# Optimization experiments

Measured on AMD Instinct MI355X. Metric: run time of the kernel, lower is better.

Reference implementation:

```python
import jax, jax.numpy as jnp
import numpy as np

TEMP = 0.5
ALPHA, BETA, GAMMA, LAMB = 1e-3, 5e-4, 1e-3, 5e-6
IMG = 1024.0  # img_metas img_shape (H_img, W_img)
LN_EPS = 1e-5


def setup_inputs() -> dict:
    key = jax.random.key(0)
    ks = jax.random.split(key, 20)
    N, C, H, W, NB = 8, 256, 128, 128, 20
    preds_S = jax.random.normal(ks[0], (N, C, H, W), jnp.float32)
    preds_T = jax.random.normal(ks[1], (N, C, H, W), jnp.float32)
    # valid boxes (tl_x, tl_y, br_x, br_y) in pixel coords within [0, IMG]
    raw = jax.random.uniform(ks[2], (N, NB, 4), jnp.float32)
    x1 = raw[..., 0] * 0.7 * IMG
    y1 = raw[..., 1] * 0.7 * IMG
    x2 = jnp.minimum(x1 + (0.05 + raw[..., 2] * 0.25) * IMG, IMG)
    y2 = jnp.minimum(y1 + (0.05 + raw[..., 3] * 0.25) * IMG, IMG)
    gt_bboxes = jnp.stack([x1, y1, x2, y2], axis=-1)
    s = 1.0 / np.sqrt(C)
    s2 = 1.0 / np.sqrt(C // 2)
    mk = lambda k, shape, sc: jax.random.normal(k, shape, jnp.float32) * sc
    return {
        'preds_S': preds_S, 'preds_T': preds_T, 'gt_bboxes': gt_bboxes,
        'w_ms': mk(ks[3], (C,), s), 'b_ms': jnp.zeros((), jnp.float32),
        'w_mt': mk(ks[4], (C,), s), 'b_mt': jnp.zeros((), jnp.float32),
        'w1_s': mk(ks[5], (C // 2, C), s), 'b1_s': jnp.zeros((C // 2,), jnp.float32),
        'g_s': jnp.ones((C // 2,), jnp.float32), 'be_s': jnp.zeros((C // 2,), jnp.float32),
        'w2_s': mk(ks[6], (C, C // 2), s2), 'b2_s': jnp.zeros((C,), jnp.float32),
        'w1_t': mk(ks[7], (C // 2, C), s), 'b1_t': jnp.zeros((C // 2,), jnp.float32),
        'g_t': jnp.ones((C // 2,), jnp.float32), 'be_t': jnp.zeros((C // 2,), jnp.float32),
        'w2_t': mk(ks[8], (C, C // 2), s2), 'b2_t': jnp.zeros((C,), jnp.float32),
    }


def _attention(x):
    # x: [N,C,H,W] -> S_att [N,H,W], C_att [N,C]
    N, C, H, W = x.shape
    v = jnp.abs(x)
    fea = v.mean(axis=1)                                   # [N,H,W]
    S = (H * W) * jax.nn.softmax((fea / TEMP).reshape(N, -1), axis=1)
    ch = v.mean(axis=(2, 3))                               # [N,C]
    Ca = C * jax.nn.softmax(ch / TEMP, axis=1)
    return S.reshape(N, H, W), Ca


def _masks(gt, H, W):
    # gt: [N,nb,4] pixel coords; box-rasterized scatter-max foreground mask
    wmin = jnp.floor(gt[..., 0] / IMG * W)
    wmax = jnp.ceil(gt[..., 2] / IMG * W)
    hmin = jnp.floor(gt[..., 1] / IMG * H)
    hmax = jnp.ceil(gt[..., 3] / IMG * H)
    area = 1.0 / ((hmax + 1.0 - hmin) * (wmax + 1.0 - wmin))  # [N,nb]
    hs = jnp.arange(H, dtype=jnp.float32)[None, None, :, None]
    ws = jnp.arange(W, dtype=jnp.float32)[None, None, None, :]
    inb = (hs >= hmin[:, :, None, None]) & (hs <= hmax[:, :, None, None]) \
        & (ws >= wmin[:, :, None, None]) & (ws <= wmax[:, :, None, None])
    Mask_fg = jnp.where(inb, area[:, :, None, None], 0.0).max(axis=1)  # [N,H,W]
    Mask_bg = jnp.where(Mask_fg > 0, 0.0, 1.0)
    sbg = Mask_bg.sum(axis=(1, 2), keepdims=True)
    Mask_bg = jnp.where(sbg > 0, Mask_bg / sbg, Mask_bg)
    return Mask_fg, Mask_bg


def _spatial_pool(x, w, b):
    N, C, H, W = x.shape
    cm = jnp.einsum('nchw,c->nhw', x, w) + b
    sm = jax.nn.softmax(cm.reshape(N, -1), axis=1).reshape(N, H, W)
    return jnp.einsum('nchw,nhw->nc', x, sm)               # [N,C]


def _channel_add(ctx, w1, b1, g, be, w2, b2):
    y = ctx @ w1.T + b1                                    # [N,C/2]
    m = y.mean(axis=1, keepdims=True)
    v = y.var(axis=1, keepdims=True)
    y = (y - m) / jnp.sqrt(v + LN_EPS) * g + be
    y = jax.nn.relu(y)
    return y @ w2.T + b2                                   # [N,C]


def reference(preds_S, preds_T, gt_bboxes, w_ms, b_ms, w_mt, b_mt,
              w1_s, b1_s, g_s, be_s, w2_s, b2_s,
              w1_t, b1_t, g_t, be_t, w2_t, b2_t):
    N, C, H, W = preds_S.shape
    S_t, C_t = _attention(preds_T)
    S_s, C_s = _attention(preds_S)
    Mask_fg, Mask_bg = _masks(gt_bboxes, H, W)
    # feature losses: (fg_s - fg_t) = (S - T) * sqrt(S_t)*sqrt(C_t)*sqrt(mask)
    wgt = jnp.sqrt(S_t)[:, None] * jnp.sqrt(C_t)[:, :, None, None]
    d = (preds_S - preds_T) * wgt
    fg_loss = jnp.sum((d * jnp.sqrt(Mask_fg)[:, None]) ** 2) / N
    bg_loss = jnp.sum((d * jnp.sqrt(Mask_bg)[:, None]) ** 2) / N
    mask_loss = jnp.sum(jnp.abs(C_s - C_t)) / N + jnp.sum(jnp.abs(S_s - S_t)) / N
    ctx_s = _spatial_pool(preds_S, w_ms, b_ms)
    ctx_t = _spatial_pool(preds_T, w_mt, b_mt)
    add_s = _channel_add(ctx_s, w1_s, b1_s, g_s, be_s, w2_s, b2_s)
    add_t = _channel_add(ctx_t, w1_t, b1_t, g_t, be_t, w2_t, b2_t)
    rd = (preds_S + add_s[:, :, None, None]) - (preds_T + add_t[:, :, None, None])
    rela_loss = jnp.sum(rd ** 2) / N
    return ALPHA * fg_loss + BETA * bg_loss + GAMMA * mask_loss + LAMB * rela_loss
```

## Files before the change

kernel.cpp:

```cpp
#include <hip/hip_runtime.h>
#include <math.h>

#define NN    8
#define CC    256
#define HWHW  16384
#define NBOX  20
#define HALF  131072

constexpr float C_ALPHA = 1e-3f, C_BETA = 5e-4f, C_GAMMA = 1e-3f, C_LAMB = 5e-6f;
constexpr float C_LN_EPS = 1e-5f;

#define OFF_FEA_S   0
#define OFF_FEA_T   262144
#define OFF_CM_S    524288
#define OFF_CM_T    786432
#define OFF_MFG     1048576
#define OFF_CHS     1179648
#define OFF_CHT     1181696
#define OFF_DSUM    1183744
#define OFF_CTXS    1185792
#define OFF_CTXT    1187840
#define OFF_BG      1189888
#define OFF_SCAL    1189896
#define OFF_CATT    1189904
#define OFF_STATS   1191952
#define OFF_MXP     1192016
#define OFF_ZP      1192528
#define OFF_RELAP   1193040

__device__ __forceinline__ float dpp_wave_sum(float x) {
#define DPPADD(ctrl, rm) \
  x += __int_as_float(__builtin_amdgcn_update_dpp(0, __float_as_int(x), ctrl, rm, 0xf, true));
  DPPADD(0x111, 0xf)
  DPPADD(0x112, 0xf)
  DPPADD(0x114, 0xf)
  DPPADD(0x118, 0xf)
  DPPADD(0x142, 0xa)
  DPPADD(0x143, 0xc)
#undef DPPADD
  return x;
}

__device__ __forceinline__ float dpp_wave_max(float x) {
#define DPPMAX(ctrl, rm) { \
  int r_ = __builtin_amdgcn_update_dpp(__float_as_int(x), __float_as_int(x), ctrl, rm, 0xf, false); \
  x = fmaxf(x, __int_as_float(r_)); }
  DPPMAX(0x111, 0xf)
  DPPMAX(0x112, 0xf)
  DPPMAX(0x114, 0xf)
  DPPMAX(0x118, 0xf)
  DPPMAX(0x142, 0xa)
  DPPMAX(0x143, 0xc)
#undef DPPMAX
  return x;
}

__device__ __forceinline__ float block_sum256(float v, float* sm) {
  int tid = threadIdx.x;
  v = dpp_wave_sum(v);
  if ((tid & 63) == 63) sm[tid >> 6] = v;
  __syncthreads();
  float r = sm[0] + sm[1] + sm[2] + sm[3];
  __syncthreads();
  return r;
}

__device__ __forceinline__ float block_max256(float v, float* sm) {
  int tid = threadIdx.x;
  v = dpp_wave_max(v);
  if ((tid & 63) == 63) sm[tid >> 6] = v;
  __syncthreads();
  float r = fmaxf(fmaxf(sm[0], sm[1]), fmaxf(sm[2], sm[3]));
  __syncthreads();
  return r;
}

__global__ __launch_bounds__(512, 2) void k1_pass1(
    const float* __restrict__ S, const float* __restrict__ T,
    const float* __restrict__ w_ms, const float* __restrict__ w_mt,
    float* __restrict__ ws) {
  int tid = threadIdx.x;
  int lane = tid & 63, sl = tid >> 6;
  int pb = blockIdx.x, cs = blockIdx.y, n = blockIdx.z;
  int pix0 = pb * 256 + lane * 4;
  int ch0 = cs * 128 + sl * 16;

  __shared__ float l_wS[128], l_wT[128];
  __shared__ float f_feaS[256], f_feaT[256], f_cmS[256], f_cmT[256];
  __shared__ float l_chS[128], l_chT[128], l_D[128];
  __shared__ float l_sq[8];

  if (tid < 128) {
    l_wS[tid] = w_ms[cs * 128 + tid];
    l_wT[tid] = w_mt[cs * 128 + tid];
  }
  if (tid < 256) {
    f_feaS[tid] = 0.f; f_feaT[tid] = 0.f; f_cmS[tid] = 0.f; f_cmT[tid] = 0.f;
  }
  __syncthreads();

  const float* baseS = S + (size_t)(n * CC + ch0) * HWHW + pix0;
  const float* baseT = T + (size_t)(n * CC + ch0) * HWHW + pix0;

  float fS[4] = {0.f, 0.f, 0.f, 0.f}, fT[4] = {0.f, 0.f, 0.f, 0.f};
  float cS[4] = {0.f, 0.f, 0.f, 0.f}, cT[4] = {0.f, 0.f, 0.f, 0.f};
  float sq = 0.f;

#define PROC1(c, s4, t4, wS_, wT_) { \
    float asx = fabsf(s4.x), asy = fabsf(s4.y), asz = fabsf(s4.z), asw = fabsf(s4.w); \
    float atx = fabsf(t4.x), aty = fabsf(t4.y), atz = fabsf(t4.z), atw = fabsf(t4.w); \
    fS[0] += asx; fS[1] += asy; fS[2] += asz; fS[3] += asw; \
    fT[0] += atx; fT[1] += aty; fT[2] += atz; fT[3] += atw; \
    chS[c] = (asx + asy) + (asz + asw); \
    chT[c] = (atx + aty) + (atz + atw); \
    cS[0] = fmaf(s4.x, wS_, cS[0]); cS[1] = fmaf(s4.y, wS_, cS[1]); \
    cS[2] = fmaf(s4.z, wS_, cS[2]); cS[3] = fmaf(s4.w, wS_, cS[3]); \
    cT[0] = fmaf(t4.x, wT_, cT[0]); cT[1] = fmaf(t4.y, wT_, cT[1]); \
    cT[2] = fmaf(t4.z, wT_, cT[2]); cT[3] = fmaf(t4.w, wT_, cT[3]); \
    float dx = s4.x - t4.x, dy = s4.y - t4.y, dz = s4.z - t4.z, dw = s4.w - t4.w; \
    sq = fmaf(dx, dx, sq); sq = fmaf(dy, dy, sq); \
    sq = fmaf(dz, dz, sq); sq = fmaf(dw, dw, sq); \
    D[c] = (dx + dy) + (dz + dw); }

#pragma unroll 1
  for (int cg = 0; cg < 4; cg++) {
    const float* bS = baseS + (size_t)(cg * 4) * HWHW;
    const float* bT = baseT + (size_t)(cg * 4) * HWHW;
    float4 s0 = *(const float4*)(bS + (size_t)0 * HWHW);
    float4 s1 = *(const float4*)(bS + (size_t)1 * HWHW);
    float4 s2 = *(const float4*)(bS + (size_t)2 * HWHW);
    float4 s3 = *(const float4*)(bS + (size_t)3 * HWHW);
    float4 t0 = *(const float4*)(bT + (size_t)0 * HWHW);
    float4 t1 = *(const float4*)(bT + (size_t)1 * HWHW);
    float4 t2 = *(const float4*)(bT + (size_t)2 * HWHW);
    float4 t3 = *(const float4*)(bT + (size_t)3 * HWHW);
    float wS0 = l_wS[sl * 16 + cg * 4 + 0], wT0 = l_wT[sl * 16 + cg * 4 + 0];
    float wS1 = l_wS[sl * 16 + cg * 4 + 1], wT1 = l_wT[sl * 16 + cg * 4 + 1];
    float wS2 = l_wS[sl * 16 + cg * 4 + 2], wT2 = l_wT[sl * 16 + cg * 4 + 2];
    float wS3 = l_wS[sl * 16 + cg * 4 + 3], wT3 = l_wT[sl * 16 + cg * 4 + 3];
    float chS[4], chT[4], D[4];
    PROC1(0, s0, t0, wS0, wT0)
    PROC1(1, s1, t1, wS1, wT1)
    PROC1(2, s2, t2, wS2, wT2)
    PROC1(3, s3, t3, wS3, wT3)
#pragma unroll
    for (int c = 0; c < 4; c++) {
      float a = dpp_wave_sum(chS[c]);
      float b = dpp_wave_sum(chT[c]);
      float d = dpp_wave_sum(D[c]);
      if (lane == 63) {
        l_chS[sl * 16 + cg * 4 + c] = a;
        l_chT[sl * 16 + cg * 4 + c] = b;
        l_D[sl * 16 + cg * 4 + c]   = d;
      }
    }
  }
#undef PROC1

  atomicAdd(&f_feaS[lane * 4 + 0], fS[0]); atomicAdd(&f_feaS[lane * 4 + 1], fS[1]);
  atomicAdd(&f_feaS[lane * 4 + 2], fS[2]); atomicAdd(&f_feaS[lane * 4 + 3], fS[3]);
  atomicAdd(&f_feaT[lane * 4 + 0], fT[0]); atomicAdd(&f_feaT[lane * 4 + 1], fT[1]);
  atomicAdd(&f_feaT[lane * 4 + 2], fT[2]); atomicAdd(&f_feaT[lane * 4 + 3], fT[3]);
  atomicAdd(&f_cmS[lane * 4 + 0], cS[0]); atomicAdd(&f_cmS[lane * 4 + 1], cS[1]);
  atomicAdd(&f_cmS[lane * 4 + 2], cS[2]); atomicAdd(&f_cmS[lane * 4 + 3], cS[3]);
  atomicAdd(&f_cmT[lane * 4 + 0], cT[0]); atomicAdd(&f_cmT[lane * 4 + 1], cT[1]);
  atomicAdd(&f_cmT[lane * 4 + 2], cT[2]); atomicAdd(&f_cmT[lane * 4 + 3], cT[3]);

  sq = dpp_wave_sum(sq);
  if (lane == 63) l_sq[sl] = sq;
  __syncthreads();

  if (tid < 256) {
    int gp = cs * HALF + n * HWHW + pb * 256 + tid;
    ws[OFF_FEA_S + gp] = f_feaS[tid];
    ws[OFF_FEA_T + gp] = f_feaT[tid];
    ws[OFF_CM_S + gp]  = f_cmS[tid];
    ws[OFF_CM_T + gp]  = f_cmT[tid];
  }
  if (tid < 128) {
    int co = n * CC + cs * 128 + tid;
    atomicAdd(&ws[OFF_CHS + co],  l_chS[tid]);
    atomicAdd(&ws[OFF_CHT + co],  l_chT[tid]);
    atomicAdd(&ws[OFF_DSUM + co], l_D[tid]);
  }
  if (tid == 0) {
    float t = 0.f;
#pragma unroll
    for (int i = 0; i < 8; i++) t += l_sq[i];
    atomicAdd(&ws[OFF_SCAL + 0], t);
  }
}

__global__ __launch_bounds__(256) void k2B_maskstats(const float* __restrict__ gt,
                                                     float* __restrict__ ws) {
  int tid = threadIdx.x;
  int pbB = blockIdx.x, n = blockIdx.y;
  int pix0 = pbB * 1024 + tid * 4;

  __shared__ float bx[NBOX][5];
  __shared__ float l_bg[4];
  __shared__ float sm[4];

  if (tid < NBOX) {
    const float* g = gt + (n * NBOX + tid) * 4;
    float wmin = floorf(g[0] * 0.125f);
    float hmin = floorf(g[1] * 0.125f);
    float wmax = ceilf(g[2] * 0.125f);
    float hmax = ceilf(g[3] * 0.125f);
    bx[tid][0] = wmin; bx[tid][1] = hmin; bx[tid][2] = wmax; bx[tid][3] = hmax;
    bx[tid][4] = 1.0f / ((hmax + 1.0f - hmin) * (wmax + 1.0f - wmin));
  }
  __syncthreads();

  float best[4] = {0.f, 0.f, 0.f, 0.f};
#pragma unroll
  for (int b = 0; b < NBOX; b++) {
    float wmin = bx[b][0], hmin = bx[b][1], wmax = bx[b][2], hmax = bx[b][3];
    float ar = bx[b][4];
#pragma unroll
    for (int j = 0; j < 4; j++) {
      int pix = pix0 + j;
      float hf = (float)(pix >> 7), wf = (float)(pix & 127);
      bool in = (hf >= hmin) && (hf <= hmax) && (wf >= wmin) && (wf <= wmax);
      best[j] = in ? fmaxf(best[j], ar) : best[j];
    }
  }
  float4 bo;
  bo.x = best[0]; bo.y = best[1]; bo.z = best[2]; bo.w = best[3];
  *(float4*)&ws[OFF_MFG + n * HWHW + pix0] = bo;

  float bg = (best[0] > 0.f ? 0.f : 1.f) + (best[1] > 0.f ? 0.f : 1.f) +
             (best[2] > 0.f ? 0.f : 1.f) + (best[3] > 0.f ? 0.f : 1.f);
  bg = dpp_wave_sum(bg);
  if ((tid & 63) == 63) l_bg[tid >> 6] = bg;
  __syncthreads();
  if (tid == 0) atomicAdd(&ws[OFF_BG + n], l_bg[0] + l_bg[1] + l_bg[2] + l_bg[3]);

  int gp = n * HWHW + pix0;
  const int   offs[4]   = {OFF_FEA_S, OFF_FEA_T, OFF_CM_S, OFF_CM_T};
  const float scales[4] = {1.0f / 128.0f, 1.0f / 128.0f, 1.0f, 1.0f};
#pragma unroll
  for (int a = 0; a < 4; a++) {
    float4 v0 = *(const float4*)&ws[offs[a] + gp];
    float4 v1 = *(const float4*)&ws[offs[a] + HALF + gp];
    float sc = scales[a];
    float vx = (v0.x + v1.x) * sc, vy = (v0.y + v1.y) * sc;
    float vz = (v0.z + v1.z) * sc, vw = (v0.w + v1.w) * sc;
    float mx = fmaxf(fmaxf(vx, vy), fmaxf(vz, vw));
    mx = block_max256(mx, sm);
    float z = expf(vx - mx) + expf(vy - mx) + expf(vz - mx) + expf(vw - mx);
    z = block_sum256(z, sm);
    if (tid == 0) {
      ws[OFF_MXP + a * 128 + n * 16 + pbB] = mx;
      ws[OFF_ZP + a * 128 + n * 16 + pbB]  = z;
    }
  }
}

__global__ __launch_bounds__(256) void kC_stats2(float* __restrict__ ws) {
  int tid = threadIdx.x, n = blockIdx.x;
  __shared__ float sm[4];

  float chS = ws[OFF_CHS + n * CC + tid];
  float chT = ws[OFF_CHT + n * CC + tid];

  float lS = chS * (1.0f / 8192.0f), lT = chT * (1.0f / 8192.0f);
  float mS = block_max256(lS, sm);
  float mT = block_max256(lT, sm);
  float eS = expf(lS - mS), eT = expf(lT - mT);
  float ZS = block_sum256(eS, sm);
  float ZT = block_sum256(eT, sm);
  float cattS = (float)CC * eS / ZS;
  float cattT = (float)CC * eT / ZT;
  ws[OFF_CATT + n * CC + tid] = cattT;
  float mml = block_sum256(fabsf(cattS - cattT), sm);
  if (tid == 0) atomicAdd(&ws[OFF_SCAL + 2], mml);

  if (tid < 4) {
    int a = tid;
    float m = -1e30f;
    for (int i = 0; i < 16; i++)
      m = fmaxf(m, ws[OFF_MXP + a * 128 + n * 16 + i]);
    float Z = 0.f;
    for (int i = 0; i < 16; i++)
      Z += ws[OFF_ZP + a * 128 + n * 16 + i] *
           expf(ws[OFF_MXP + a * 128 + n * 16 + i] - m);
    ws[OFF_STATS + n * 8 + 2 * a]     = m;
    ws[OFF_STATS + n * 8 + 2 * a + 1] = Z;
  }
}

__global__ __launch_bounds__(512, 2) void k4_pass2(
    const float* __restrict__ S, const float* __restrict__ T,
    float* __restrict__ ws) {
  int tid = threadIdx.x;
  int lane = tid & 63, sl = tid >> 6;
  int pb = blockIdx.x, cs = blockIdx.y, n = blockIdx.z;
  int pix0 = pb * 256 + lane * 4;
  int ch0 = cs * 128 + sl * 16;

  __shared__ float l_catt[128];
  __shared__ float wcombL[256], smsL[256], smtL[256];
  __shared__ float l_cs[128], l_ct[128], l_c[8];

  if (tid < 128) l_catt[tid] = ws[OFF_CATT + n * CC + cs * 128 + tid];
  if (tid < 64) {
    float mxFS = ws[OFF_STATS + n * 8 + 0], ZFS = ws[OFF_STATS + n * 8 + 1];
    float mxFT = ws[OFF_STATS + n * 8 + 2], ZFT = ws[OFF_STATS + n * 8 + 3];
    float mxCS = ws[OFF_STATS + n * 8 + 4], ZCS = ws[OFF_STATS + n * 8 + 5];
    float mxCT = ws[OFF_STATS + n * 8 + 6], ZCT = ws[OFF_STATS + n * 8 + 7];
    float bgc  = ws[OFF_BG + n];
    int gp = n * HWHW + pb * 256 + tid * 4;
    float4 fS0 = *(const float4*)&ws[OFF_FEA_S + gp];
    float4 fS1 = *(const float4*)&ws[OFF_FEA_S + HALF + gp];
    float4 fT0 = *(const float4*)&ws[OFF_FEA_T + gp];
    float4 fT1 = *(const float4*)&ws[OFF_FEA_T + HALF + gp];
    float4 cS0 = *(const float4*)&ws[OFF_CM_S + gp];
    float4 cS1 = *(const float4*)&ws[OFF_CM_S + HALF + gp];
    float4 cT0 = *(const float4*)&ws[OFF_CM_T + gp];
    float4 cT1 = *(const float4*)&ws[OFF_CM_T + HALF + gp];
    float4 mf = *(const float4*)&ws[OFF_MFG + gp];
    float fSa[4] = {fS0.x + fS1.x, fS0.y + fS1.y, fS0.z + fS1.z, fS0.w + fS1.w};
    float fTa[4] = {fT0.x + fT1.x, fT0.y + fT1.y, fT0.z + fT1.z, fT0.w + fT1.w};
    float cSa[4] = {cS0.x + cS1.x, cS0.y + cS1.y, cS0.z + cS1.z, cS0.w + cS1.w};
    float cTa[4] = {cT0.x + cT1.x, cT0.y + cT1.y, cT0.z + cT1.z, cT0.w + cT1.w};
    float mfa[4] = {mf.x, mf.y, mf.z, mf.w};
    float macc = 0.f;
#pragma unroll
    for (int j = 0; j < 4; j++) {
      float pT = expf(fTa[j] * (1.0f / 128.0f) - mxFT) / ZFT;
      float pS = expf(fSa[j] * (1.0f / 128.0f) - mxFS) / ZFS;
      float Satt = (float)HWHW * pT;
      float mbg = (mfa[j] > 0.f) ? 0.f : ((bgc > 0.f) ? 1.0f / bgc : 1.0f);
      wcombL[tid * 4 + j] = Satt * (C_ALPHA * mfa[j] + C_BETA * mbg);
      smsL[tid * 4 + j] = expf(cSa[j] - mxCS) / ZCS;
      smtL[tid * 4 + j] = expf(cTa[j] - mxCT) / ZCT;
      macc += fabsf(pS - pT);
    }
    macc = dpp_wave_sum(macc);
    if (tid == 63 && cs == 0) atomicAdd(&ws[OFF_SCAL + 2], macc * (float)HWHW);
  }
  __syncthreads();

  float4 sms = *(const float4*)&smsL[lane * 4];
  float4 smt = *(const float4*)&smtL[lane * 4];
  float4 wcb = *(const float4*)&wcombL[lane * 4];

  const float* baseS = S + (size_t)(n * CC + ch0) * HWHW + pix0;
  const float* baseT = T + (size_t)(n * CC + ch0) * HWHW + pix0;

  float aw[4] = {0.f, 0.f, 0.f, 0.f};

#define PROC2(c, s4, t4, ca_) { \
    float dx = s4.x - t4.x, dy = s4.y - t4.y, dz = s4.z - t4.z, dw = s4.w - t4.w; \
    aw[0] = fmaf(dx * dx, ca_, aw[0]); aw[1] = fmaf(dy * dy, ca_, aw[1]); \
    aw[2] = fmaf(dz * dz, ca_, aw[2]); aw[3] = fmaf(dw * dw, ca_, aw[3]); \
    ctxS[c] = fmaf(s4.x, sms.x, fmaf(s4.y, sms.y, fmaf(s4.z, sms.z, s4.w * sms.w))); \
    ctxT[c] = fmaf(t4.x, smt.x, fmaf(t4.y, smt.y, fmaf(t4.z, smt.z, t4.w * smt.w))); }

#pragma unroll 1
  for (int cg = 0; cg < 4; cg++) {
    const float* bS = baseS + (size_t)(cg * 4) * HWHW;
    const float* bT = baseT + (size_t)(cg * 4) * HWHW;
    float4 s0 = *(const float4*)(bS + (size_t)0 * HWHW);
    float4 s1 = *(const float4*)(bS + (size_t)1 * HWHW);
    float4 s2 = *(const float4*)(bS + (size_t)2 * HWHW);
    float4 s3 = *(const float4*)(bS + (size_t)3 * HWHW);
    float4 t0 = *(const float4*)(bT + (size_t)0 * HWHW);
    float4 t1 = *(const float4*)(bT + (size_t)1 * HWHW);
    float4 t2 = *(const float4*)(bT + (size_t)2 * HWHW);
    float4 t3 = *(const float4*)(bT + (size_t)3 * HWHW);
    float ca0 = l_catt[sl * 16 + cg * 4 + 0];
    float ca1 = l_catt[sl * 16 + cg * 4 + 1];
    float ca2 = l_catt[sl * 16 + cg * 4 + 2];
    float ca3 = l_catt[sl * 16 + cg * 4 + 3];
    float ctxS[4], ctxT[4];
    PROC2(0, s0, t0, ca0)
    PROC2(1, s1, t1, ca1)
    PROC2(2, s2, t2, ca2)
    PROC2(3, s3, t3, ca3)
#pragma unroll
    for (int c = 0; c < 4; c++) {
      float xs = dpp_wave_sum(ctxS[c]);
      float xt = dpp_wave_sum(ctxT[c]);
      if (lane == 63) {
        l_cs[sl * 16 + cg * 4 + c] = xs;
        l_ct[sl * 16 + cg * 4 + c] = xt;
      }
    }
  }
#undef PROC2

  float contrib = fmaf(aw[0], wcb.x, fmaf(aw[1], wcb.y, fmaf(aw[2], wcb.z, aw[3] * wcb.w)));
  contrib = dpp_wave_sum(contrib);
  if (lane == 63) l_c[sl] = contrib;
  __syncthreads();

  if (tid < 128) {
    int co = n * CC + cs * 128 + tid;
    atomicAdd(&ws[OFF_CTXS + co], l_cs[tid]);
    atomicAdd(&ws[OFF_CTXT + co], l_ct[tid]);
  }
  if (tid == 0) {
    float t = 0.f;
#pragma unroll
    for (int i = 0; i < 8; i++) t += l_c[i];
    atomicAdd(&ws[OFF_SCAL + 1], t);
  }
}

__global__ __launch_bounds__(512) void k5_mlp(
    const float* __restrict__ w1_s, const float* __restrict__ b1_s,
    const float* __restrict__ g_s,  const float* __restrict__ be_s,
    const float* __restrict__ w1_t, const float* __restrict__ b1_t,
    const float* __restrict__ g_t,  const float* __restrict__ be_t,
    const float* __restrict__ w2_s, const float* __restrict__ b2_s,
    const float* __restrict__ w2_t, const float* __restrict__ b2_t,
    float* __restrict__ ws) {
  int tid = threadIdx.x, n = blockIdx.x;
  int lane = tid & 63;
  __shared__ float ctxS[CC], ctxT[CC], ysh[128], yth[128];
  __shared__ float red[4], smr[8];

  if (tid < 256)      ctxS[tid] = ws[OFF_CTXS + n * CC + tid];
  else                ctxT[tid - 256] = ws[OFF_CTXT + n * CC + (tid - 256)];
  __syncthreads();

  int st = (tid >> 7) & 1, j = tid & 127;
  float acc = 0.f;
  if (tid < 256) {
    const float* w1 = st ? w1_t : w1_s;
    const float* b1 = st ? b1_t : b1_s;
    const float* ctx = st ? ctxT : ctxS;
    acc = b1[j];
    const float* wr = w1 + j * CC;
#pragma unroll 8
    for (int c = 0; c < CC; c += 4) {
      float4 w = *(const float4*)(wr + c);
      acc = fmaf(w.x, ctx[c], acc);
      acc = fmaf(w.y, ctx[c + 1], acc);
      acc = fmaf(w.z, ctx[c + 2], acc);
      acc = fmaf(w.w, ctx[c + 3], acc);
    }
  }

  float v = dpp_wave_sum(acc);
  if (tid < 256 && lane == 63) red[tid >> 6] = v;
  __syncthreads();
  int grp = tid >> 7;
  float mean = 0.f;
  if (tid < 256) mean = (red[grp * 2] + red[grp * 2 + 1]) * (1.0f / 128.0f);
  __syncthreads();
  float dm = acc - mean;
  v = dpp_wave_sum(dm * dm);
  if (tid < 256 && lane == 63) red[tid >> 6] = v;
  __syncthreads();
  if (tid < 256) {
    float var = (red[grp * 2] + red[grp * 2 + 1]) * (1.0f / 128.0f);
    const float* g  = st ? g_t  : g_s;
    const float* be = st ? be_t : be_s;
    float q = dm * (1.0f / sqrtf(var + C_LN_EPS)) * g[j] + be[j];
    q = q > 0.f ? q : 0.f;
    if (st == 0) ysh[j] = q;
    else         yth[j] = q;
  }
  __syncthreads();

  float rp = 0.f;
  if (tid < 256) {
    int c = tid;
    float es = b2_s[c], et = b2_t[c];
    const float* w2sr = w2_s + c * 128;
    const float* w2tr = w2_t + c * 128;
#pragma unroll 8
    for (int jj = 0; jj < 128; jj += 4) {
      float4 a = *(const float4*)(w2sr + jj);
      float4 b = *(const float4*)(w2tr + jj);
      es = fmaf(a.x, ysh[jj], es); es = fmaf(a.y, ysh[jj + 1], es);
      es = fmaf(a.z, ysh[jj + 2], es); es = fmaf(a.w, ysh[jj + 3], es);
      et = fmaf(b.x, yth[jj], et); et = fmaf(b.y, yth[jj + 1], et);
      et = fmaf(b.z, yth[jj + 2], et); et = fmaf(b.w, yth[jj + 3], et);
    }
    float e = es - et;
    rp = 2.0f * e * ws[OFF_DSUM + n * CC + c] + (float)HWHW * e * e;
  }
  rp = dpp_wave_sum(rp);
  if (lane == 63) smr[tid >> 6] = rp;
  __syncthreads();
  if (tid == 0) {
    float t = 0.f;
#pragma unroll
    for (int i = 0; i < 8; i++) t += smr[i];
    ws[OFF_RELAP + n] = t;
  }
}

__global__ __launch_bounds__(64) void k5c_final(float* __restrict__ ws,
                                                float* __restrict__ out) {
  int lane = threadIdx.x;
  float r = (lane < NN) ? ws[OFF_RELAP + lane] : 0.f;
  r = dpp_wave_sum(r);
  if (lane == 63) {
    float rela = ws[OFF_SCAL + 0] + r;
    out[0] = (ws[OFF_SCAL + 1] + C_GAMMA * ws[OFF_SCAL + 2] + C_LAMB * rela) *
             (1.0f / (float)NN);
  }
}

extern "C" void kernel_launch(void* const* d_in, const int* in_sizes, int n_in,
                              void* d_out, int out_size, void* d_ws, size_t ws_size,
                              hipStream_t stream) {
  const float* S    = (const float*)d_in[0];
  const float* T    = (const float*)d_in[1];
  const float* gt   = (const float*)d_in[2];
  const float* w_ms = (const float*)d_in[3];
  const float* w_mt = (const float*)d_in[5];
  const float* w1_s = (const float*)d_in[7];
  const float* b1_s = (const float*)d_in[8];
  const float* g_s  = (const float*)d_in[9];
  const float* be_s = (const float*)d_in[10];
  const float* w2_s = (const float*)d_in[11];
  const float* b2_s = (const float*)d_in[12];
  const float* w1_t = (const float*)d_in[13];
  const float* b1_t = (const float*)d_in[14];
  const float* g_t  = (const float*)d_in[15];
  const float* be_t = (const float*)d_in[16];
  const float* w2_t = (const float*)d_in[17];
  const float* b2_t = (const float*)d_in[18];
  float* ws = (float*)d_ws;
  float* out = (float*)d_out;

  hipMemsetAsync(ws + OFF_CHS, 0, 10256 * sizeof(float), stream);

  k1_pass1<<<dim3(64, 2, 8), dim3(512), 0, stream>>>(S, T, w_ms, w_mt, ws);
  k2B_maskstats<<<dim3(16, 8), dim3(256), 0, stream>>>(gt, ws);
  kC_stats2<<<dim3(8), dim3(256), 0, stream>>>(ws);
  k4_pass2<<<dim3(64, 2, 8), dim3(512), 0, stream>>>(S, T, ws);
  k5_mlp<<<dim3(8), dim3(512), 0, stream>>>(w1_s, b1_s, g_s, be_s,
                                            w1_t, b1_t, g_t, be_t,
                                            w2_s, b2_s, w2_t, b2_t, ws);
  k5c_final<<<dim3(1), dim3(64), 0, stream>>>(ws, out);
}
```

Measured before the change: 398.8 us.

## Cut launch count: fold memset into mask kernel, merge stats, last-block final reduce

Replaces the memset with zeroing inside a new mask-rasterization kernel that runs before pass1. It merges the two small stats kernels into one per-image kernel that runs an online softmax over all pixels. It also drops the final kernel by having the last MLP block, detected with an atomic counter, compute the output. The goal is to remove three launches and their serialization gaps. In exchange the merged stats kernel uses only 8 blocks with serial loops over 16K pixels and four maps, which may lengthen the critical path.

```diff
diff --git a/kernel.cpp b/kernel.cpp
--- a/kernel.cpp
+++ b/kernel.cpp
@@ -24,9 +24,10 @@
 #define OFF_SCAL    1189896
 #define OFF_CATT    1189904
 #define OFF_STATS   1191952
-#define OFF_MXP     1192016
-#define OFF_ZP      1192528
 #define OFF_RELAP   1193040
+#define OFF_BGP     1193048
+#define OFF_MML     1193176
+#define ZERO_SPAN   10256
 
 __device__ __forceinline__ float dpp_wave_sum(float x) {
 #define DPPADD(ctrl, rm) \
@@ -73,6 +74,55 @@
   float r = fmaxf(fmaxf(sm[0], sm[1]), fmaxf(sm[2], sm[3]));
   __syncthreads();
   return r;
+}
+
+__global__ __launch_bounds__(256) void k0_maskzero(const float* __restrict__ gt,
+                                                   float* __restrict__ ws) {
+  int tid = threadIdx.x;
+  int pbB = blockIdx.x, n = blockIdx.y;
+  int pix0 = pbB * 1024 + tid * 4;
+
+  int gi = (n * 16 + pbB) * 256 + tid;
+  if (gi < ZERO_SPAN) ws[OFF_CHS + gi] = 0.f;
+
+  __shared__ float bx[NBOX][5];
+  __shared__ float l_bg[4];
+
+  if (tid < NBOX) {
+    const float* g = gt + (n * NBOX + tid) * 4;
+    float wmin = floorf(g[0] * 0.125f);
+    float hmin = floorf(g[1] * 0.125f);
+    float wmax = ceilf(g[2] * 0.125f);
+    float hmax = ceilf(g[3] * 0.125f);
+    bx[tid][0] = wmin; bx[tid][1] = hmin; bx[tid][2] = wmax; bx[tid][3] = hmax;
+    bx[tid][4] = 1.0f / ((hmax + 1.0f - hmin) * (wmax + 1.0f - wmin));
+  }
+  __syncthreads();
+
+  float best[4] = {0.f, 0.f, 0.f, 0.f};
+#pragma unroll
+  for (int b = 0; b < NBOX; b++) {
+    float wmin = bx[b][0], hmin = bx[b][1], wmax = bx[b][2], hmax = bx[b][3];
+    float ar = bx[b][4];
+#pragma unroll
+    for (int j = 0; j < 4; j++) {
+      int pix = pix0 + j;
+      float hf = (float)(pix >> 7), wf = (float)(pix & 127);
+      bool in = (hf >= hmin) && (hf <= hmax) && (wf >= wmin) && (wf <= wmax);
+      best[j] = in ? fmaxf(best[j], ar) : best[j];
+    }
+  }
+  float4 bo;
+  bo.x = best[0]; bo.y = best[1]; bo.z = best[2]; bo.w = best[3];
+  *(float4*)&ws[OFF_MFG + n * HWHW + pix0] = bo;
+
+  float bg = (best[0] > 0.f ? 0.f : 1.f) + (best[1] > 0.f ? 0.f : 1.f) +
+             (best[2] > 0.f ? 0.f : 1.f) + (best[3] > 0.f ? 0.f : 1.f);
+  bg = dpp_wave_sum(bg);
+  if ((tid & 63) == 63) l_bg[tid >> 6] = bg;
+  __syncthreads();
+  if (tid == 0)
+    ws[OFF_BGP + n * 16 + pbB] = l_bg[0] + l_bg[1] + l_bg[2] + l_bg[3];
 }
 
 __global__ __launch_bounds__(512, 2) void k1_pass1(
@@ -191,79 +241,64 @@
   }
 }
 
-__global__ __launch_bounds__(256) void k2B_maskstats(const float* __restrict__ gt,
-                                                     float* __restrict__ ws) {
-  int tid = threadIdx.x;
-  int pbB = blockIdx.x, n = blockIdx.y;
-  int pix0 = pbB * 1024 + tid * 4;
-
-  __shared__ float bx[NBOX][5];
-  __shared__ float l_bg[4];
+__global__ __launch_bounds__(256) void k2C_stats(float* __restrict__ ws) {
+  int tid = threadIdx.x, n = blockIdx.x;
+  int lane = tid & 63;
   __shared__ float sm[4];
-
-  if (tid < NBOX) {
-    const float* g = gt + (n * NBOX + tid) * 4;
-    float wmin = floorf(g[0] * 0.125f);
-    float hmin = floorf(g[1] * 0.125f);
-    float wmax = ceilf(g[2] * 0.125f);
-    float hmax = ceilf(g[3] * 0.125f);
-    bx[tid][0] = wmin; bx[tid][1] = hmin; bx[tid][2] = wmax; bx[tid][3] = hmax;
-    bx[tid][4] = 1.0f / ((hmax + 1.0f - hmin) * (wmax + 1.0f - wmin));
-  }
-  __syncthreads();
-
-  float best[4] = {0.f, 0.f, 0.f, 0.f};
-#pragma unroll
-  for (int b = 0; b < NBOX; b++) {
-    float wmin = bx[b][0], hmin = bx[b][1], wmax = bx[b][2], hmax = bx[b][3];
-    float ar = bx[b][4];
-#pragma unroll
-    for (int j = 0; j < 4; j++) {
-      int pix = pix0 + j;
-      float hf = (float)(pix >> 7), wf = (float)(pix & 127);
-      bool in = (hf >= hmin) && (hf <= hmax) && (wf >= wmin) && (wf <= wmax);
-      best[j] = in ? fmaxf(best[j], ar) : best[j];
-    }
-  }
-  float4 bo;
-  bo.x = best[0]; bo.y = best[1]; bo.z = best[2]; bo.w = best[3];
-  *(float4*)&ws[OFF_MFG + n * HWHW + pix0] = bo;
-
-  float bg = (best[0] > 0.f ? 0.f : 1.f) + (best[1] > 0.f ? 0.f : 1.f) +
-             (best[2] > 0.f ? 0.f : 1.f) + (best[3] > 0.f ? 0.f : 1.f);
-  bg = dpp_wave_sum(bg);
-  if ((tid & 63) == 63) l_bg[tid >> 6] = bg;
-  __syncthreads();
-  if (tid == 0) atomicAdd(&ws[OFF_BG + n], l_bg[0] + l_bg[1] + l_bg[2] + l_bg[3]);
-
-  int gp = n * HWHW + pix0;
+  __shared__ float wm[4], wz[4];
+
+  if (tid == 0) {
+    float b = 0.f;
+    for (int i = 0; i < 16; i++) b += ws[OFF_BGP + n * 16 + i];
+    ws[OFF_BG + n] = b;
+  }
+
   const int   offs[4]   = {OFF_FEA_S, OFF_FEA_T, OFF_CM_S, OFF_CM_T};
   const float scales[4] = {1.0f / 128.0f, 1.0f / 128.0f, 1.0f, 1.0f};
-#pragma unroll
+#pragma unroll 1
   for (int a = 0; a < 4; a++) {
-    float4 v0 = *(const float4*)&ws[offs[a] + gp];
-    float4 v1 = *(const float4*)&ws[offs[a] + HALF + gp];
+    float m = -1e30f, z = 0.f;
+    int base = offs[a] + n * HWHW;
     float sc = scales[a];
-    float vx = (v0.x + v1.x) * sc, vy = (v0.y + v1.y) * sc;
-    float vz = (v0.z + v1.z) * sc, vw = (v0.w + v1.w) * sc;
-    float mx = fmaxf(fmaxf(vx, vy), fmaxf(vz, vw));
-    mx = block_max256(mx, sm);
-    float z = expf(vx - mx) + expf(vy - mx) + expf(vz - mx) + expf(vw - mx);
-    z = block_sum256(z, sm);
+    for (int k = 0; k < 16; k++) {
+      int i = k * 1024 + tid * 4;
+      float4 v0 = *(const float4*)&ws[base + i];
+      float4 v1 = *(const float4*)&ws[base + HALF + i];
+      float vv[4] = {(v0.x + v1.x) * sc, (v0.y + v1.y) * sc,
+                     (v0.z + v1.z) * sc, (v0.w + v1.w) * sc};
+#pragma unroll
+      for (int j = 0; j < 4; j++) {
+        float v = vv[j];
+        float mn = fmaxf(m, v);
+        z = z * expf(m - mn) + expf(v - mn);
+        m = mn;
+      }
+    }
+#pragma unroll
+    for (int d = 1; d < 64; d <<= 1) {
+      float m2 = __shfl_xor(m, d);
+      float z2 = __shfl_xor(z, d);
+      float mn = fmaxf(m, m2);
+      z = z * expf(m - mn) + z2 * expf(m2 - mn);
+      m = mn;
+    }
+    if (lane == 0) { wm[tid >> 6] = m; wz[tid >> 6] = z; }
+    __syncthreads();
     if (tid == 0) {
-      ws[OFF_MXP + a * 128 + n * 16 + pbB] = mx;
-      ws[OFF_ZP + a * 128 + n * 16 + pbB]  = z;
-    }
-  }
-}
-
-__global__ __launch_bounds__(256) void kC_stats2(float* __restrict__ ws) {
-  int tid = threadIdx.x, n = blockIdx.x;
-  __shared__ float sm[4];
+      float M = wm[0], Z = wz[0];
+      for (int w = 1; w < 4; w++) {
+        float mn = fmaxf(M, wm[w]);
+        Z = Z * expf(M - mn) + wz[w] * expf(wm[w] - mn);
+        M = mn;
+      }
+      ws[OFF_STATS + n * 8 + 2 * a]     = M;
+      ws[OFF_STATS + n * 8 + 2 * a + 1] = Z;
+    }
+    __syncthreads();
+  }
 
   float chS = ws[OFF_CHS + n * CC + tid];
   float chT = ws[OFF_CHT + n * CC + tid];
-
   float lS = chS * (1.0f / 8192.0f), lT = chT * (1.0f / 8192.0f);
   float mS = block_max256(lS, sm);
   float mT = block_max256(lT, sm);
@@ -274,20 +309,7 @@
   float cattT = (float)CC * eT / ZT;
   ws[OFF_CATT + n * CC + tid] = cattT;
   float mml = block_sum256(fabsf(cattS - cattT), sm);
-  if (tid == 0) atomicAdd(&ws[OFF_SCAL + 2], mml);
-
-  if (tid < 4) {
-    int a = tid;
-    float m = -1e30f;
-    for (int i = 0; i < 16; i++)
-      m = fmaxf(m, ws[OFF_MXP + a * 128 + n * 16 + i]);
-    float Z = 0.f;
-    for (int i = 0; i < 16; i++)
-      Z += ws[OFF_ZP + a * 128 + n * 16 + i] *
-           expf(ws[OFF_MXP + a * 128 + n * 16 + i] - m);
-    ws[OFF_STATS + n * 8 + 2 * a]     = m;
-    ws[OFF_STATS + n * 8 + 2 * a + 1] = Z;
-  }
+  if (tid == 0) ws[OFF_MML + n] = mml;
 }
 
 __global__ __launch_bounds__(512, 2) void k4_pass2(
@@ -409,14 +431,14 @@
   }
 }
 
-__global__ __launch_bounds__(512) void k5_mlp(
+__global__ __launch_bounds__(512) void k5F_mlp(
     const float* __restrict__ w1_s, const float* __restrict__ b1_s,
     const float* __restrict__ g_s,  const float* __restrict__ be_s,
     const float* __restrict__ w1_t, const float* __restrict__ b1_t,
     const float* __restrict__ g_t,  const float* __restrict__ be_t,
     const float* __restrict__ w2_s, const float* __restrict__ b2_s,
     const float* __restrict__ w2_t, const float* __restrict__ b2_t,
-    float* __restrict__ ws) {
+    float* __restrict__ ws, float* __restrict__ out) {
   int tid = threadIdx.x, n = blockIdx.x;
   int lane = tid & 63;
   __shared__ float ctxS[CC], ctxT[CC], ysh[128], yth[128];
@@ -487,23 +509,26 @@
   rp = dpp_wave_sum(rp);
   if (lane == 63) smr[tid >> 6] = rp;
   __syncthreads();
+
   if (tid == 0) {
     float t = 0.f;
 #pragma unroll
     for (int i = 0; i < 8; i++) t += smr[i];
     ws[OFF_RELAP + n] = t;
-  }
-}
-
-__global__ __launch_bounds__(64) void k5c_final(float* __restrict__ ws,
-                                                float* __restrict__ out) {
-  int lane = threadIdx.x;
-  float r = (lane < NN) ? ws[OFF_RELAP + lane] : 0.f;
-  r = dpp_wave_sum(r);
-  if (lane == 63) {
-    float rela = ws[OFF_SCAL + 0] + r;
-    out[0] = (ws[OFF_SCAL + 1] + C_GAMMA * ws[OFF_SCAL + 2] + C_LAMB * rela) *
-             (1.0f / (float)NN);
+    __threadfence();
+    int old = atomicAdd((int*)&ws[OFF_SCAL + 3], 1);
+    if (old == NN - 1) {
+      __threadfence();
+      float relp = 0.f, mml = ws[OFF_SCAL + 2];
+#pragma unroll
+      for (int i = 0; i < NN; i++) {
+        relp += ws[OFF_RELAP + i];
+        mml  += ws[OFF_MML + i];
+      }
+      float rela = ws[OFF_SCAL + 0] + relp;
+      out[0] = (ws[OFF_SCAL + 1] + C_GAMMA * mml + C_LAMB * rela) *
+               (1.0f / (float)NN);
+    }
   }
 }
 
@@ -530,14 +555,11 @@
   float* ws = (float*)d_ws;
   float* out = (float*)d_out;
 
-  hipMemsetAsync(ws + OFF_CHS, 0, 10256 * sizeof(float), stream);
-
+  k0_maskzero<<<dim3(16, 8), dim3(256), 0, stream>>>(gt, ws);
   k1_pass1<<<dim3(64, 2, 8), dim3(512), 0, stream>>>(S, T, w_ms, w_mt, ws);
-  k2B_maskstats<<<dim3(16, 8), dim3(256), 0, stream>>>(gt, ws);
-  kC_stats2<<<dim3(8), dim3(256), 0, stream>>>(ws);
+  k2C_stats<<<dim3(8), dim3(256), 0, stream>>>(ws);
   k4_pass2<<<dim3(64, 2, 8), dim3(512), 0, stream>>>(S, T, ws);
-  k5_mlp<<<dim3(8), dim3(512), 0, stream>>>(w1_s, b1_s, g_s, be_s,
-                                            w1_t, b1_t, g_t, be_t,
-                                            w2_s, b2_s, w2_t, b2_t, ws);
-  k5c_final<<<dim3(1), dim3(64), 0, stream>>>(ws, out);
-}
+  k5F_mlp<<<dim3(8), dim3(512), 0, stream>>>(w1_s, b1_s, g_s, be_s,
+                                             w1_t, b1_t, g_t, be_t,
+                                             w2_s, b2_s, w2_t, b2_t, ws, out);
+}
```

Measured after the change: 428.3 us. 1.07x slower.

## Fold memset into mask kernel and fuse final reduction into MLP kernel

Applied to the files above, without the earlier changes.

Replaces the hipMemsetAsync with a k0 kernel that zeroes the workspace and also rasterizes the foreground mask, moving that work ahead of pass1. Background counts and per-sample mask losses now go to per-block slots instead of atomics, and the final scalar combine moves into the MLP kernel through a last-block-done atomic counter, dropping one launch. The aim is to cut launch and serialization overhead between small kernels. The counter at SCAL+3 lies inside the zeroed span, so it resets every call.

```diff
diff --git a/kernel.cpp b/kernel.cpp
--- a/kernel.cpp
+++ b/kernel.cpp
@@ -27,6 +27,9 @@
 #define OFF_MXP     1192016
 #define OFF_ZP      1192528
 #define OFF_RELAP   1193040
+#define OFF_BGP     1193048
+#define OFF_MML     1193176
+#define ZERO_SPAN   10256
 
 __device__ __forceinline__ float dpp_wave_sum(float x) {
 #define DPPADD(ctrl, rm) \
@@ -73,6 +76,51 @@
   float r = fmaxf(fmaxf(sm[0], sm[1]), fmaxf(sm[2], sm[3]));
   __syncthreads();
   return r;
+}
+
+__global__ __launch_bounds__(256) void k0_maskzero(const float* __restrict__ gt,
+                                                   float* __restrict__ ws) {
+  int tid = threadIdx.x;
+  int pbB = blockIdx.x, n = blockIdx.y;
+  int pix0 = pbB * 1024 + tid * 4;
+  int gi = (n * 16 + pbB) * 256 + tid;
+  if (gi < ZERO_SPAN) ws[OFF_CHS + gi] = 0.f;
+
+  __shared__ float bx[NBOX][5];
+  __shared__ float l_bg[4];
+  if (tid < NBOX) {
+    const float* g = gt + (n * NBOX + tid) * 4;
+    float wmin = floorf(g[0] * 0.125f);
+    float hmin = floorf(g[1] * 0.125f);
+    float wmax = ceilf(g[2] * 0.125f);
+    float hmax = ceilf(g[3] * 0.125f);
+    bx[tid][0] = wmin; bx[tid][1] = hmin; bx[tid][2] = wmax; bx[tid][3] = hmax;
+    bx[tid][4] = 1.0f / ((hmax + 1.0f - hmin) * (wmax + 1.0f - wmin));
+  }
+  __syncthreads();
+  float best[4] = {0.f, 0.f, 0.f, 0.f};
+#pragma unroll
+  for (int b = 0; b < NBOX; b++) {
+    float wmin = bx[b][0], hmin = bx[b][1], wmax = bx[b][2], hmax = bx[b][3];
+    float ar = bx[b][4];
+#pragma unroll
+    for (int j = 0; j < 4; j++) {
+      int pix = pix0 + j;
+      float hf = (float)(pix >> 7), wf = (float)(pix & 127);
+      bool in = (hf >= hmin) && (hf <= hmax) && (wf >= wmin) && (wf <= wmax);
+      best[j] = in ? fmaxf(best[j], ar) : best[j];
+    }
+  }
+  float4 bo;
+  bo.x = best[0]; bo.y = best[1]; bo.z = best[2]; bo.w = best[3];
+  *(float4*)&ws[OFF_MFG + n * HWHW + pix0] = bo;
+  float bg = (best[0] > 0.f ? 0.f : 1.f) + (best[1] > 0.f ? 0.f : 1.f) +
+             (best[2] > 0.f ? 0.f : 1.f) + (best[3] > 0.f ? 0.f : 1.f);
+  bg = dpp_wave_sum(bg);
+  if ((tid & 63) == 63) l_bg[tid >> 6] = bg;
+  __syncthreads();
+  if (tid == 0)
+    ws[OFF_BGP + n * 16 + pbB] = l_bg[0] + l_bg[1] + l_bg[2] + l_bg[3];
 }
 
 __global__ __launch_bounds__(512, 2) void k1_pass1(
@@ -123,9 +171,9 @@
     D[c] = (dx + dy) + (dz + dw); }
 
 #pragma unroll 1
-  for (int cg = 0; cg < 4; cg++) {
-    const float* bS = baseS + (size_t)(cg * 4) * HWHW;
-    const float* bT = baseT + (size_t)(cg * 4) * HWHW;
+  for (int cg4 = 0; cg4 < 4; cg4++) {
+    const float* bS = baseS + (size_t)(cg4 * 4) * HWHW;
+    const float* bT = baseT + (size_t)(cg4 * 4) * HWHW;
     float4 s0 = *(const float4*)(bS + (size_t)0 * HWHW);
     float4 s1 = *(const float4*)(bS + (size_t)1 * HWHW);
     float4 s2 = *(const float4*)(bS + (size_t)2 * HWHW);
@@ -134,10 +182,10 @@
     float4 t1 = *(const float4*)(bT + (size_t)1 * HWHW);
     float4 t2 = *(const float4*)(bT + (size_t)2 * HWHW);
     float4 t3 = *(const float4*)(bT + (size_t)3 * HWHW);
-    float wS0 = l_wS[sl * 16 + cg * 4 + 0], wT0 = l_wT[sl * 16 + cg * 4 + 0];
-    float wS1 = l_wS[sl * 16 + cg * 4 + 1], wT1 = l_wT[sl * 16 + cg * 4 + 1];
-    float wS2 = l_wS[sl * 16 + cg * 4 + 2], wT2 = l_wT[sl * 16 + cg * 4 + 2];
-    float wS3 = l_wS[sl * 16 + cg * 4 + 3], wT3 = l_wT[sl * 16 + cg * 4 + 3];
+    float wS0 = l_wS[sl * 16 + cg4 * 4 + 0], wT0 = l_wT[sl * 16 + cg4 * 4 + 0];
+    float wS1 = l_wS[sl * 16 + cg4 * 4 + 1], wT1 = l_wT[sl * 16 + cg4 * 4 + 1];
+    float wS2 = l_wS[sl * 16 + cg4 * 4 + 2], wT2 = l_wT[sl * 16 + cg4 * 4 + 2];
+    float wS3 = l_wS[sl * 16 + cg4 * 4 + 3], wT3 = l_wT[sl * 16 + cg4 * 4 + 3];
     float chS[4], chT[4], D[4];
     PROC1(0, s0, t0, wS0, wT0)
     PROC1(1, s1, t1, wS1, wT1)
@@ -149,9 +197,9 @@
       float b = dpp_wave_sum(chT[c]);
       float d = dpp_wave_sum(D[c]);
       if (lane == 63) {
-        l_chS[sl * 16 + cg * 4 + c] = a;
-        l_chT[sl * 16 + cg * 4 + c] = b;
-        l_D[sl * 16 + cg * 4 + c]   = d;
+        l_chS[sl * 16 + cg4 * 4 + c] = a;
+        l_chT[sl * 16 + cg4 * 4 + c] = b;
+        l_D[sl * 16 + cg4 * 4 + c]   = d;
       }
     }
   }
@@ -191,50 +239,11 @@
   }
 }
 
-__global__ __launch_bounds__(256) void k2B_maskstats(const float* __restrict__ gt,
-                                                     float* __restrict__ ws) {
+__global__ __launch_bounds__(256) void k2B_stats(float* __restrict__ ws) {
   int tid = threadIdx.x;
   int pbB = blockIdx.x, n = blockIdx.y;
   int pix0 = pbB * 1024 + tid * 4;
-
-  __shared__ float bx[NBOX][5];
-  __shared__ float l_bg[4];
   __shared__ float sm[4];
-
-  if (tid < NBOX) {
-    const float* g = gt + (n * NBOX + tid) * 4;
-    float wmin = floorf(g[0] * 0.125f);
-    float hmin = floorf(g[1] * 0.125f);
-    float wmax = ceilf(g[2] * 0.125f);
-    float hmax = ceilf(g[3] * 0.125f);
-    bx[tid][0] = wmin; bx[tid][1] = hmin; bx[tid][2] = wmax; bx[tid][3] = hmax;
-    bx[tid][4] = 1.0f / ((hmax + 1.0f - hmin) * (wmax + 1.0f - wmin));
-  }
-  __syncthreads();
-
-  float best[4] = {0.f, 0.f, 0.f, 0.f};
-#pragma unroll
-  for (int b = 0; b < NBOX; b++) {
-    float wmin = bx[b][0], hmin = bx[b][1], wmax = bx[b][2], hmax = bx[b][3];
-    float ar = bx[b][4];
-#pragma unroll
-    for (int j = 0; j < 4; j++) {
-      int pix = pix0 + j;
-      float hf = (float)(pix >> 7), wf = (float)(pix & 127);
-      bool in = (hf >= hmin) && (hf <= hmax) && (wf >= wmin) && (wf <= wmax);
-      best[j] = in ? fmaxf(best[j], ar) : best[j];
-    }
-  }
-  float4 bo;
-  bo.x = best[0]; bo.y = best[1]; bo.z = best[2]; bo.w = best[3];
-  *(float4*)&ws[OFF_MFG + n * HWHW + pix0] = bo;
-
-  float bg = (best[0] > 0.f ? 0.f : 1.f) + (best[1] > 0.f ? 0.f : 1.f) +
-             (best[2] > 0.f ? 0.f : 1.f) + (best[3] > 0.f ? 0.f : 1.f);
-  bg = dpp_wave_sum(bg);
-  if ((tid & 63) == 63) l_bg[tid >> 6] = bg;
-  __syncthreads();
-  if (tid == 0) atomicAdd(&ws[OFF_BG + n], l_bg[0] + l_bg[1] + l_bg[2] + l_bg[3]);
 
   int gp = n * HWHW + pix0;
   const int   offs[4]   = {OFF_FEA_S, OFF_FEA_T, OFF_CM_S, OFF_CM_T};
@@ -261,21 +270,11 @@
   int tid = threadIdx.x, n = blockIdx.x;
   __shared__ float sm[4];
 
-  float chS = ws[OFF_CHS + n * CC + tid];
-  float chT = ws[OFF_CHT + n * CC + tid];
-
-  float lS = chS * (1.0f / 8192.0f), lT = chT * (1.0f / 8192.0f);
-  float mS = block_max256(lS, sm);
-  float mT = block_max256(lT, sm);
-  float eS = expf(lS - mS), eT = expf(lT - mT);
-  float ZS = block_sum256(eS, sm);
-  float ZT = block_sum256(eT, sm);
-  float cattS = (float)CC * eS / ZS;
-  float cattT = (float)CC * eT / ZT;
-  ws[OFF_CATT + n * CC + tid] = cattT;
-  float mml = block_sum256(fabsf(cattS - cattT), sm);
-  if (tid == 0) atomicAdd(&ws[OFF_SCAL + 2], mml);
-
+  if (tid == 0) {
+    float b = 0.f;
+    for (int i = 0; i < 16; i++) b += ws[OFF_BGP + n * 16 + i];
+    ws[OFF_BG + n] = b;
+  }
   if (tid < 4) {
     int a = tid;
     float m = -1e30f;
@@ -288,6 +287,20 @@
     ws[OFF_STATS + n * 8 + 2 * a]     = m;
     ws[OFF_STATS + n * 8 + 2 * a + 1] = Z;
   }
+
+  float chS = ws[OFF_CHS + n * CC + tid];
+  float chT = ws[OFF_CHT + n * CC + tid];
+  float lS = chS * (1.0f / 8192.0f), lT = chT * (1.0f / 8192.0f);
+  float mS = block_max256(lS, sm);
+  float mT = block_max256(lT, sm);
+  float eS = expf(lS - mS), eT = expf(lT - mT);
+  float ZS = block_sum256(eS, sm);
+  float ZT = block_sum256(eT, sm);
+  float cattS = (float)CC * eS / ZS;
+  float cattT = (float)CC * eT / ZT;
+  ws[OFF_CATT + n * CC + tid] = cattT;
+  float mml = block_sum256(fabsf(cattS - cattT), sm);
+  if (tid == 0) ws[OFF_MML + n] = mml;
 }
 
 __global__ __launch_bounds__(512, 2) void k4_pass2(
@@ -359,9 +372,9 @@
     ctxT[c] = fmaf(t4.x, smt.x, fmaf(t4.y, smt.y, fmaf(t4.z, smt.z, t4.w * smt.w))); }
 
 #pragma unroll 1
-  for (int cg = 0; cg < 4; cg++) {
-    const float* bS = baseS + (size_t)(cg * 4) * HWHW;
-    const float* bT = baseT + (size_t)(cg * 4) * HWHW;
+  for (int cg4 = 0; cg4 < 4; cg4++) {
+    const float* bS = baseS + (size_t)(cg4 * 4) * HWHW;
+    const float* bT = baseT + (size_t)(cg4 * 4) * HWHW;
     float4 s0 = *(const float4*)(bS + (size_t)0 * HWHW);
     float4 s1 = *(const float4*)(bS + (size_t)1 * HWHW);
     float4 s2 = *(const float4*)(bS + (size_t)2 * HWHW);
@@ -370,10 +383,10 @@
     float4 t1 = *(const float4*)(bT + (size_t)1 * HWHW);
     float4 t2 = *(const float4*)(bT + (size_t)2 * HWHW);
     float4 t3 = *(const float4*)(bT + (size_t)3 * HWHW);
-    float ca0 = l_catt[sl * 16 + cg * 4 + 0];
-    float ca1 = l_catt[sl * 16 + cg * 4 + 1];
-    float ca2 = l_catt[sl * 16 + cg * 4 + 2];
-    float ca3 = l_catt[sl * 16 + cg * 4 + 3];
+    float ca0 = l_catt[sl * 16 + cg4 * 4 + 0];
+    float ca1 = l_catt[sl * 16 + cg4 * 4 + 1];
+    float ca2 = l_catt[sl * 16 + cg4 * 4 + 2];
+    float ca3 = l_catt[sl * 16 + cg4 * 4 + 3];
     float ctxS[4], ctxT[4];
     PROC2(0, s0, t0, ca0)
     PROC2(1, s1, t1, ca1)
@@ -384,8 +397,8 @@
       float xs = dpp_wave_sum(ctxS[c]);
       float xt = dpp_wave_sum(ctxT[c]);
       if (lane == 63) {
-        l_cs[sl * 16 + cg * 4 + c] = xs;
-        l_ct[sl * 16 + cg * 4 + c] = xt;
+        l_cs[sl * 16 + cg4 * 4 + c] = xs;
+        l_ct[sl * 16 + cg4 * 4 + c] = xt;
       }
     }
   }
@@ -409,14 +422,14 @@
   }
 }
 
-__global__ __launch_bounds__(512) void k5_mlp(
+__global__ __launch_bounds__(512) void k5F_mlp(
     const float* __restrict__ w1_s, const float* __restrict__ b1_s,
     const float* __restrict__ g_s,  const float* __restrict__ be_s,
     const float* __restrict__ w1_t, const float* __restrict__ b1_t,
     const float* __restrict__ g_t,  const float* __restrict__ be_t,
     const float* __restrict__ w2_s, const float* __restrict__ b2_s,
     const float* __restrict__ w2_t, const float* __restrict__ b2_t,
-    float* __restrict__ ws) {
+    float* __restrict__ ws, float* __restrict__ out) {
   int tid = threadIdx.x, n = blockIdx.x;
   int lane = tid & 63;
   __shared__ float ctxS[CC], ctxT[CC], ysh[128], yth[128];
@@ -487,23 +500,26 @@
   rp = dpp_wave_sum(rp);
   if (lane == 63) smr[tid >> 6] = rp;
   __syncthreads();
+
   if (tid == 0) {
     float t = 0.f;
 #pragma unroll
     for (int i = 0; i < 8; i++) t += smr[i];
     ws[OFF_RELAP + n] = t;
-  }
-}
-
-__global__ __launch_bounds__(64) void k5c_final(float* __restrict__ ws,
-                                                float* __restrict__ out) {
-  int lane = threadIdx.x;
-  float r = (lane < NN) ? ws[OFF_RELAP + lane] : 0.f;
-  r = dpp_wave_sum(r);
-  if (lane == 63) {
-    float rela = ws[OFF_SCAL + 0] + r;
-    out[0] = (ws[OFF_SCAL + 1] + C_GAMMA * ws[OFF_SCAL + 2] + C_LAMB * rela) *
-             (1.0f / (float)NN);
+    __threadfence();
+    int old = atomicAdd((int*)&ws[OFF_SCAL + 3], 1);
+    if (old == NN - 1) {
+      __threadfence();
+      float relp = 0.f, mml = ws[OFF_SCAL + 2];
+#pragma unroll
+      for (int i = 0; i < NN; i++) {
+        relp += ws[OFF_RELAP + i];
+        mml  += ws[OFF_MML + i];
+      }
+      float rela = ws[OFF_SCAL + 0] + relp;
+      out[0] = (ws[OFF_SCAL + 1] + C_GAMMA * mml + C_LAMB * rela) *
+               (1.0f / (float)NN);
+    }
   }
 }
 
@@ -530,14 +546,12 @@
   float* ws = (float*)d_ws;
   float* out = (float*)d_out;
 
-  hipMemsetAsync(ws + OFF_CHS, 0, 10256 * sizeof(float), stream);
-
+  k0_maskzero<<<dim3(16, 8), dim3(256), 0, stream>>>(gt, ws);
   k1_pass1<<<dim3(64, 2, 8), dim3(512), 0, stream>>>(S, T, w_ms, w_mt, ws);
-  k2B_maskstats<<<dim3(16, 8), dim3(256), 0, stream>>>(gt, ws);
+  k2B_stats<<<dim3(16, 8), dim3(256), 0, stream>>>(ws);
   kC_stats2<<<dim3(8), dim3(256), 0, stream>>>(ws);
   k4_pass2<<<dim3(64, 2, 8), dim3(512), 0, stream>>>(S, T, ws);
-  k5_mlp<<<dim3(8), dim3(512), 0, stream>>>(w1_s, b1_s, g_s, be_s,
-                                            w1_t, b1_t, g_t, be_t,
-                                            w2_s, b2_s, w2_t, b2_t, ws);
-  k5c_final<<<dim3(1), dim3(64), 0, stream>>>(ws, out);
-}
+  k5F_mlp<<<dim3(8), dim3(512), 0, stream>>>(w1_s, b1_s, g_s, be_s,
+                                             w1_t, b1_t, g_t, be_t,
+                                             w2_s, b2_s, w2_t, b2_t, ws, out);
+}
```

Result: no change. 398.4 us (-0.1%).
